# Kernel tuning notes

Measured on AMD Instinct MI355X. Metric: run time of the kernel, lower is better.

Reference implementation:

```python
import jax, jax.numpy as jnp
import numpy as np

N_NODES = 40000
N_EDGES = 640000
N_FEAT = 128
HIDDEN = 128
N_GRAPHS = 64


def _sage_conv(x, src, dst, Wl, b, Wr):
    # PyG SAGEConv (aggr='mean', root_weight=True, normalize=False):
    # out_i = W_l @ mean_{j in N(i)} x_j + b + W_r @ x_i
    msg = x[src]                                             # [E, F]
    s = jax.ops.segment_sum(msg, dst, num_segments=N_NODES)  # [N, F]
    deg = jax.ops.segment_sum(jnp.ones((src.shape[0],), x.dtype), dst,
                              num_segments=N_NODES)
    agg = s / jnp.maximum(deg, 1.0)[:, None]
    return agg @ Wl + b + x @ Wr


def setup_inputs() -> dict:
    key = jax.random.key(0)
    ks = jax.random.split(key, 12)
    sc = 1.0 / np.sqrt(N_FEAT)
    x = jax.random.normal(ks[0], (N_NODES, N_FEAT), dtype=jnp.float32)
    edge_index = jax.random.randint(ks[1], (2, N_EDGES), 0, N_NODES, dtype=jnp.int32)
    batch = jnp.sort(jax.random.randint(ks[2], (N_NODES,), 0, N_GRAPHS, dtype=jnp.int32))
    mk = lambda k, shp: (jax.random.normal(k, shp, dtype=jnp.float32) * sc)
    return {
        'x': x, 'edge_index': edge_index, 'batch': batch,
        'W1l': mk(ks[3], (N_FEAT, HIDDEN)), 'b1': jnp.zeros((HIDDEN,), jnp.float32),
        'W1r': mk(ks[4], (N_FEAT, HIDDEN)),
        'W2l': mk(ks[5], (HIDDEN, HIDDEN)), 'b2': jnp.zeros((HIDDEN,), jnp.float32),
        'W2r': mk(ks[6], (HIDDEN, HIDDEN)),
        'W3l': mk(ks[7], (HIDDEN, HIDDEN)), 'b3': jnp.zeros((HIDDEN,), jnp.float32),
        'W3r': mk(ks[8], (HIDDEN, HIDDEN)),
        'Wlin': mk(ks[9], (3 * HIDDEN, HIDDEN)), 'blin': jnp.zeros((HIDDEN,), jnp.float32),
    }


def reference(x, edge_index, batch, W1l, b1, W1r, W2l, b2, W2r, W3l, b3, W3r, Wlin, blin):
    src, dst = edge_index[0], edge_index[1]
    h1 = jax.nn.relu(_sage_conv(x, src, dst, W1l, b1, W1r))
    h2 = jax.nn.relu(_sage_conv(h1, src, dst, W2l, b2, W2r))
    h3 = jax.nn.relu(_sage_conv(h2, src, dst, W3l, b3, W3r))
    h = jnp.concatenate([h1, h2, h3], axis=1)                # [N, 3*H]
    pooled = jax.ops.segment_sum(h, batch, num_segments=N_GRAPHS)  # global_add_pool
    out = jax.nn.relu(pooled @ Wlin + blin)                  # [G, H]
    return out
```

## Files before the change

kernel.cpp:

```cpp
#include <hip/hip_runtime.h>
#include <hip/hip_bf16.h>

#define N_NODES 40000
#define N_EDGES 640000
#define NFEAT 128
#define NGRAPHS 64
#define ECAP 1536

typedef __attribute__((ext_vector_type(8))) short short8;
typedef __attribute__((ext_vector_type(4))) float float4v;

static __device__ __forceinline__ float bf2f(unsigned short u) {
    unsigned int x = ((unsigned int)u) << 16;
    return __builtin_bit_cast(float, x);
}
static __device__ __forceinline__ unsigned short f2bf(float f) {
    unsigned int x = __builtin_bit_cast(unsigned int, f);
    unsigned int r = x + 0x7fffu + ((x >> 16) & 1u);
    return (unsigned short)(r >> 16);
}

__global__ void k_prep(const int* __restrict__ dst, int* __restrict__ deg,
                       const int* __restrict__ batch, int* __restrict__ goff,
                       const float* __restrict__ x, unsigned short* __restrict__ h0,
                       const float* __restrict__ Wl0, const float* __restrict__ Wr0,
                       const float* __restrict__ Wl1, const float* __restrict__ Wr1,
                       const float* __restrict__ Wl2, const float* __restrict__ Wr2,
                       unsigned short* __restrict__ Wt) {
    int b = blockIdx.x;
    if (b < 2500) {
        int e = b * 256 + threadIdx.x;
        if (e < N_EDGES) atomicAdd(&deg[dst[e]], 1);
    } else if (b < 2657) {
        int i = (b - 2500) * 256 + threadIdx.x;
        if (i >= N_NODES) return;
        int b1 = batch[i];
        int b0 = (i == 0) ? -1 : batch[i - 1];
        for (int g = b0 + 1; g <= b1; ++g) goff[g] = i;
        if (i == N_NODES - 1)
            for (int g = b1 + 1; g <= NGRAPHS; ++g) goff[g] = N_NODES;
    } else if (b < 12657) {
        int i = (b - 2657) * 256 + threadIdx.x;
        const int n = N_NODES * NFEAT / 2;
        if (i < n) {
            float a = x[2 * i], c = x[2 * i + 1];
            unsigned int u = (unsigned int)f2bf(a) | ((unsigned int)f2bf(c) << 16);
            ((unsigned int*)h0)[i] = u;
        }
    } else {
        int id = (b - 12657) * 256 + threadIdx.x;
        if (id >= 3 * 128 * 256) return;
        int l   = id >> 15;
        int rem = id & 32767;
        int nn  = rem >> 8;
        int k   = rem & 255;
        const float* Wl = (l == 0) ? Wl0 : (l == 1) ? Wl1 : Wl2;
        const float* Wr = (l == 0) ? Wr0 : (l == 1) ? Wr1 : Wr2;
        float v = (k < 128) ? Wl[k * 128 + nn] : Wr[(k - 128) * 128 + nn];
        Wt[id] = f2bf(v);
    }
}

__global__ __launch_bounds__(1024) void k_scan1(const int* __restrict__ deg,
                                                int* __restrict__ offsets,
                                                int* __restrict__ bsum) {
    __shared__ int ws[16];
    int tid = threadIdx.x;
    int i = blockIdx.x * 1024 + tid;
    int v = (i < N_NODES) ? deg[i] : 0;
    int lane = tid & 63, wave = tid >> 6;
    int incl = v;
    for (int d = 1; d < 64; d <<= 1) {
        int t = __shfl_up(incl, d, 64);
        if (lane >= d) incl += t;
    }
    if (lane == 63) ws[wave] = incl;
    __syncthreads();
    if (wave == 0 && lane < 16) {
        int w = ws[lane];
        for (int d = 1; d < 16; d <<= 1) {
            int t = __shfl_up(w, d, 64);
            if (lane >= d) w += t;
        }
        ws[lane] = w;
    }
    __syncthreads();
    int waveOff = (wave == 0) ? 0 : ws[wave - 1];
    if (i < N_NODES) offsets[i] = waveOff + incl - v;
    if (tid == 1023) bsum[blockIdx.x] = ws[15];
}

__global__ __launch_bounds__(1024) void k_scan3(const int* __restrict__ bsum,
                                                int* __restrict__ offsets,
                                                int* __restrict__ cursor) {
    __shared__ int s_boff;
    int tid = threadIdx.x;
    if (tid < 64) {
        int v = (tid < 40) ? bsum[tid] : 0;
        int incl = v;
        for (int d = 1; d < 64; d <<= 1) {
            int t = __shfl_up(incl, d, 64);
            if (tid >= d) incl += t;
        }
        int excl = incl - v;
        int my = __shfl(excl, blockIdx.x, 64);
        if (tid == 0) s_boff = my;
    }
    __syncthreads();
    int boff = s_boff;
    int i = blockIdx.x * 1024 + tid;
    if (i < N_NODES) {
        int o = offsets[i] + boff;
        offsets[i] = o;
        cursor[i]  = o;
    }
    if (blockIdx.x == 0 && tid == 0) offsets[N_NODES] = N_EDGES;
}

__global__ void k_fill(const int* __restrict__ src, const int* __restrict__ dst,
                       int* __restrict__ cursor, int* __restrict__ esrc) {
    int e = blockIdx.x * 256 + threadIdx.x;
    if (e < N_EDGES) {
        int d = dst[e];
        int p = atomicAdd(&cursor[d], 1);
        esrc[p] = src[e];
    }
}

__global__ __launch_bounds__(256) void k_sage(
        const unsigned short* __restrict__ hin,
        const int* __restrict__ offsets,
        const int* __restrict__ esrc,
        const unsigned short* __restrict__ Wt,
        const float* __restrict__ bias,
        unsigned short* __restrict__ hout) {
    __shared__ __align__(16) unsigned short As[64][136];
    __shared__ int eidx[ECAP];
    int tid = threadIdx.x;
    int row0 = blockIdx.x * 64;

    int estart = offsets[row0];
    int ecnt   = offsets[row0 + 64] - estart;
    int staged = ecnt < ECAP ? ecnt : ECAP;

    for (int t = tid; t < staged; t += 256) eidx[t] = esrc[estart + t];
    __syncthreads();

    {
        int grp = tid >> 4;
        int sub = tid & 15;
        for (int nn = 0; nn < 4; ++nn) {
            int r = nn * 16 + grp;
            int node = row0 + r;
            int beg = offsets[node], end = offsets[node + 1];
            float a[8];
            for (int i = 0; i < 8; ++i) a[i] = 0.f;
            auto acc8 = [&](uint4 u) {
                a[0] += bf2f((unsigned short)(u.x & 0xffffu));
                a[1] += bf2f((unsigned short)(u.x >> 16));
                a[2] += bf2f((unsigned short)(u.y & 0xffffu));
                a[3] += bf2f((unsigned short)(u.y >> 16));
                a[4] += bf2f((unsigned short)(u.z & 0xffffu));
                a[5] += bf2f((unsigned short)(u.z >> 16));
                a[6] += bf2f((unsigned short)(u.w & 0xffffu));
                a[7] += bf2f((unsigned short)(u.w >> 16));
            };
            if (end - estart <= staged) {
                int lj = beg - estart, lend = end - estart;
                for (; lj + 8 <= lend; lj += 8) {
                    int s0 = eidx[lj],     s1 = eidx[lj + 1];
                    int s2 = eidx[lj + 2], s3 = eidx[lj + 3];
                    int s4 = eidx[lj + 4], s5 = eidx[lj + 5];
                    int s6 = eidx[lj + 6], s7 = eidx[lj + 7];
                    uint4 u0 = *(const uint4*)(hin + (size_t)s0 * 128 + sub * 8);
                    uint4 u1 = *(const uint4*)(hin + (size_t)s1 * 128 + sub * 8);
                    uint4 u2 = *(const uint4*)(hin + (size_t)s2 * 128 + sub * 8);
                    uint4 u3 = *(const uint4*)(hin + (size_t)s3 * 128 + sub * 8);
                    uint4 u4 = *(const uint4*)(hin + (size_t)s4 * 128 + sub * 8);
                    uint4 u5 = *(const uint4*)(hin + (size_t)s5 * 128 + sub * 8);
                    uint4 u6 = *(const uint4*)(hin + (size_t)s6 * 128 + sub * 8);
                    uint4 u7 = *(const uint4*)(hin + (size_t)s7 * 128 + sub * 8);
                    acc8(u0); acc8(u1); acc8(u2); acc8(u3);
                    acc8(u4); acc8(u5); acc8(u6); acc8(u7);
                }
                for (; lj < lend; ++lj) {
                    int s = eidx[lj];
                    uint4 u = *(const uint4*)(hin + (size_t)s * 128 + sub * 8);
                    acc8(u);
                }
            } else {
                for (int j = beg; j < end; ++j) {
                    int s = esrc[j];
                    uint4 u = *(const uint4*)(hin + (size_t)s * 128 + sub * 8);
                    acc8(u);
                }
            }
            int deg = end - beg;
            float inv = 1.f / (float)(deg > 1 ? deg : 1);
            uint4 v;
            v.x = (unsigned int)f2bf(a[0] * inv) | ((unsigned int)f2bf(a[1] * inv) << 16);
            v.y = (unsigned int)f2bf(a[2] * inv) | ((unsigned int)f2bf(a[3] * inv) << 16);
            v.z = (unsigned int)f2bf(a[4] * inv) | ((unsigned int)f2bf(a[5] * inv) << 16);
            v.w = (unsigned int)f2bf(a[6] * inv) | ((unsigned int)f2bf(a[7] * inv) << 16);
            *(uint4*)(&As[r][sub * 8]) = v;
        }
    }

    int wave = tid >> 6, lane = tid & 63;
    int quad = lane >> 4, l16 = lane & 15;
    float4v acc[4][2];
    for (int rt = 0; rt < 4; ++rt)
        for (int ct = 0; ct < 2; ++ct) acc[rt][ct] = {0.f, 0.f, 0.f, 0.f};

    int ncol0 = wave * 32;

    for (int kc = 0; kc < 4; ++kc) {
        int kg = kc * 32 + quad * 8;
        short8 a[4], b[2];
        for (int rt = 0; rt < 4; ++rt)
            a[rt] = *(const short8*)(hin + (size_t)(row0 + rt * 16 + l16) * 128 + kg);
        for (int ct = 0; ct < 2; ++ct)
            b[ct] = *(const short8*)(Wt + (size_t)(ncol0 + ct * 16 + l16) * 256 + 128 + kg);
        for (int rt = 0; rt < 4; ++rt)
            for (int ct = 0; ct < 2; ++ct)
                acc[rt][ct] = __builtin_amdgcn_mfma_f32_16x16x32_bf16(
                    a[rt], b[ct], acc[rt][ct], 0, 0, 0);
    }

    __syncthreads();

    for (int kc = 0; kc < 4; ++kc) {
        int k0 = kc * 32 + quad * 8;
        short8 a[4], b[2];
        for (int rt = 0; rt < 4; ++rt)
            a[rt] = *(const short8*)(&As[rt * 16 + l16][k0]);
        for (int ct = 0; ct < 2; ++ct)
            b[ct] = *(const short8*)(Wt + (size_t)(ncol0 + ct * 16 + l16) * 256 + k0);
        for (int rt = 0; rt < 4; ++rt)
            for (int ct = 0; ct < 2; ++ct)
                acc[rt][ct] = __builtin_amdgcn_mfma_f32_16x16x32_bf16(
                    a[rt], b[ct], acc[rt][ct], 0, 0, 0);
    }

    for (int ct = 0; ct < 2; ++ct) {
        int col = ncol0 + ct * 16 + l16;
        float bv = bias[col];
        for (int rt = 0; rt < 4; ++rt) {
            int r0 = rt * 16 + quad * 4;
            for (int i = 0; i < 4; ++i) {
                float v = acc[rt][ct][i] + bv;
                v = v > 0.f ? v : 0.f;
                hout[(size_t)(row0 + r0 + i) * 128 + col] = f2bf(v);
            }
        }
    }
}

__global__ __launch_bounds__(256) void k_pool(const unsigned short* __restrict__ h1,
                                              const unsigned short* __restrict__ h2,
                                              const unsigned short* __restrict__ h3,
                                              const int* __restrict__ goff,
                                              float* __restrict__ pooled) {
    __shared__ float red[4][16][8];
    int b = blockIdx.x;
    int g = b / 3, aidx = b % 3;
    const unsigned short* h = (aidx == 0) ? h1 : (aidx == 1) ? h2 : h3;
    int beg = goff[g], end = goff[g + 1];
    int tid = threadIdx.x;
    int rp = tid >> 4;
    int ch = tid & 15;
    float a[8];
    for (int i = 0; i < 8; ++i) a[i] = 0.f;
    for (int r = beg + rp; r < end; r += 16) {
        uint4 u = *(const uint4*)(h + (size_t)r * 128 + ch * 8);
        a[0] += bf2f((unsigned short)(u.x & 0xffffu));
        a[1] += bf2f((unsigned short)(u.x >> 16));
        a[2] += bf2f((unsigned short)(u.y & 0xffffu));
        a[3] += bf2f((unsigned short)(u.y >> 16));
        a[4] += bf2f((unsigned short)(u.z & 0xffffu));
        a[5] += bf2f((unsigned short)(u.z >> 16));
        a[6] += bf2f((unsigned short)(u.w & 0xffffu));
        a[7] += bf2f((unsigned short)(u.w >> 16));
    }
    for (int i = 0; i < 8; ++i) {
        a[i] += __shfl_xor(a[i], 16, 64);
        a[i] += __shfl_xor(a[i], 32, 64);
    }
    int wave = tid >> 6, lane = tid & 63;
    if (lane < 16)
        for (int i = 0; i < 8; ++i) red[wave][lane][i] = a[i];
    __syncthreads();
    if (tid < 128) {
        int ch2 = tid >> 3, e = tid & 7;
        float s = red[0][ch2][e] + red[1][ch2][e] + red[2][ch2][e] + red[3][ch2][e];
        pooled[g * 384 + aidx * 128 + ch2 * 8 + e] = s;
    }
}

__global__ void k_final(const float* __restrict__ pooled,
                        const float* __restrict__ Wlin,
                        const float* __restrict__ blin,
                        float* __restrict__ out) {
    int g = blockIdx.x, col = threadIdx.x;
    float acc = blin[col];
    for (int k = 0; k < 384; ++k)
        acc = fmaf(pooled[g * 384 + k], Wlin[k * 128 + col], acc);
    out[g * 128 + col] = acc > 0.f ? acc : 0.f;
}

extern "C" void kernel_launch(void* const* d_in, const int* in_sizes, int n_in,
                              void* d_out, int out_size, void* d_ws, size_t ws_size,
                              hipStream_t stream) {
    const float* x    = (const float*)d_in[0];
    const int*   ei   = (const int*)d_in[1];
    const int*   src  = ei;
    const int*   dst  = ei + N_EDGES;
    const int*   batch = (const int*)d_in[2];
    const float* W1l = (const float*)d_in[3];
    const float* b1  = (const float*)d_in[4];
    const float* W1r = (const float*)d_in[5];
    const float* W2l = (const float*)d_in[6];
    const float* b2  = (const float*)d_in[7];
    const float* W2r = (const float*)d_in[8];
    const float* W3l = (const float*)d_in[9];
    const float* b3  = (const float*)d_in[10];
    const float* W3r = (const float*)d_in[11];
    const float* Wlin = (const float*)d_in[12];
    const float* blin = (const float*)d_in[13];
    float* out = (float*)d_out;

    char* ws = (char*)d_ws;
    size_t off = 0;
    auto alloc = [&](size_t bytes) -> char* {
        char* p = ws + off;
        off = (off + bytes + 255) & ~(size_t)255;
        return p;
    };
    int* offsets = (int*)alloc((N_NODES + 1) * sizeof(int));
    int* cursor  = (int*)alloc(N_NODES * sizeof(int));
    int* deg     = (int*)alloc(N_NODES * sizeof(int));
    int* bsum    = (int*)alloc(64 * sizeof(int));
    int* goff    = (int*)alloc((NGRAPHS + 1) * sizeof(int));
    int* esrc    = (int*)alloc(N_EDGES * sizeof(int));
    unsigned short* h0   = (unsigned short*)alloc((size_t)N_NODES * 128 * 2);
    unsigned short* h1   = (unsigned short*)alloc((size_t)N_NODES * 128 * 2);
    unsigned short* h2   = (unsigned short*)alloc((size_t)N_NODES * 128 * 2);
    unsigned short* h3   = (unsigned short*)alloc((size_t)N_NODES * 128 * 2);
    unsigned short* Wt   = (unsigned short*)alloc(3 * 256 * 128 * 2);
    float* pooled = (float*)alloc(NGRAPHS * 384 * sizeof(float));

    hipMemsetAsync(deg, 0, N_NODES * sizeof(int), stream);

    k_prep<<<13041, 256, 0, stream>>>(dst, deg, batch, goff, x, h0,
                                      W1l, W1r, W2l, W2r, W3l, W3r, Wt);
    k_scan1<<<40, 1024, 0, stream>>>(deg, offsets, bsum);
    k_scan3<<<40, 1024, 0, stream>>>(bsum, offsets, cursor);
    k_fill<<<(N_EDGES + 255) / 256, 256, 0, stream>>>(src, dst, cursor, esrc);

    k_sage<<<625, 256, 0, stream>>>(h0, offsets, esrc, Wt,             b1, h1);
    k_sage<<<625, 256, 0, stream>>>(h1, offsets, esrc, Wt + 32768,     b2, h2);
    k_sage<<<625, 256, 0, stream>>>(h2, offsets, esrc, Wt + 2 * 32768, b3, h3);

    k_pool<<<3 * NGRAPHS, 256, 0, stream>>>(h1, h2, h3, goff, pooled);
    k_final<<<NGRAPHS, 128, 0, stream>>>(pooled, Wlin, blin, out);
}
```

Baseline: 283.6 us.

## Fuse scan kernels, stage root features in LDS, fuse pool with final linear

```diff
diff --git a/kernel.cpp b/kernel.cpp
--- a/kernel.cpp
+++ b/kernel.cpp
@@ -61,19 +61,37 @@
     }
 }
 
-__global__ __launch_bounds__(1024) void k_scan1(const int* __restrict__ deg,
-                                                int* __restrict__ offsets,
-                                                int* __restrict__ bsum) {
+__global__ __launch_bounds__(1024) void k_scan(const int* __restrict__ deg,
+                                               int* __restrict__ offsets,
+                                               int* __restrict__ cursor) {
     __shared__ int ws[16];
+    __shared__ int s_boff;
     int tid = threadIdx.x;
-    int i = blockIdx.x * 1024 + tid;
+    int b = blockIdx.x;
+    int lane = tid & 63, wave = tid >> 6;
+
+    int lim = b << 10;
+    int s = 0;
+    for (int i = tid; i < lim; i += 1024) s += deg[i];
+    for (int d = 1; d < 64; d <<= 1) s += __shfl_xor(s, d, 64);
+    if (lane == 0) ws[wave] = s;
+    __syncthreads();
+    if (tid == 0) {
+        int t = 0;
+        for (int w = 0; w < 16; ++w) t += ws[w];
+        s_boff = t;
+    }
+    __syncthreads();
+    int boff = s_boff;
+
+    int i = (b << 10) + tid;
     int v = (i < N_NODES) ? deg[i] : 0;
-    int lane = tid & 63, wave = tid >> 6;
     int incl = v;
     for (int d = 1; d < 64; d <<= 1) {
         int t = __shfl_up(incl, d, 64);
         if (lane >= d) incl += t;
     }
+    __syncthreads();
     if (lane == 63) ws[wave] = incl;
     __syncthreads();
     if (wave == 0 && lane < 16) {
@@ -86,35 +104,12 @@
     }
     __syncthreads();
     int waveOff = (wave == 0) ? 0 : ws[wave - 1];
-    if (i < N_NODES) offsets[i] = waveOff + incl - v;
-    if (tid == 1023) bsum[blockIdx.x] = ws[15];
-}
-
-__global__ __launch_bounds__(1024) void k_scan3(const int* __restrict__ bsum,
-                                                int* __restrict__ offsets,
-                                                int* __restrict__ cursor) {
-    __shared__ int s_boff;
-    int tid = threadIdx.x;
-    if (tid < 64) {
-        int v = (tid < 40) ? bsum[tid] : 0;
-        int incl = v;
-        for (int d = 1; d < 64; d <<= 1) {
-            int t = __shfl_up(incl, d, 64);
-            if (tid >= d) incl += t;
-        }
-        int excl = incl - v;
-        int my = __shfl(excl, blockIdx.x, 64);
-        if (tid == 0) s_boff = my;
-    }
-    __syncthreads();
-    int boff = s_boff;
-    int i = blockIdx.x * 1024 + tid;
     if (i < N_NODES) {
-        int o = offsets[i] + boff;
+        int o = boff + waveOff + incl - v;
         offsets[i] = o;
         cursor[i]  = o;
     }
-    if (blockIdx.x == 0 && tid == 0) offsets[N_NODES] = N_EDGES;
+    if (b == 39 && tid == 0) offsets[N_NODES] = N_EDGES;
 }
 
 __global__ void k_fill(const int* __restrict__ src, const int* __restrict__ dst,
@@ -134,7 +129,7 @@
         const unsigned short* __restrict__ Wt,
         const float* __restrict__ bias,
         unsigned short* __restrict__ hout) {
-    __shared__ __align__(16) unsigned short As[64][136];
+    __shared__ __align__(16) unsigned short As[64][264];
     __shared__ int eidx[ECAP];
     int tid = threadIdx.x;
     int row0 = blockIdx.x * 64;
@@ -143,6 +138,12 @@
     int ecnt   = offsets[row0 + 64] - estart;
     int staged = ecnt < ECAP ? ecnt : ECAP;
 
+    for (int p = 0; p < 4; ++p) {
+        int ci = tid + p * 256;
+        int r = ci >> 4, c8 = ci & 15;
+        uint4 v = *(const uint4*)(hin + (size_t)(row0 + r) * 128 + c8 * 8);
+        *(uint4*)(&As[r][128 + c8 * 8]) = v;
+    }
     for (int t = tid; t < staged; t += 256) eidx[t] = esrc[estart + t];
     __syncthreads();
 
@@ -205,6 +206,7 @@
             *(uint4*)(&As[r][sub * 8]) = v;
         }
     }
+    __syncthreads();
 
     int wave = tid >> 6, lane = tid & 63;
     int quad = lane >> 4, l16 = lane & 15;
@@ -213,23 +215,7 @@
         for (int ct = 0; ct < 2; ++ct) acc[rt][ct] = {0.f, 0.f, 0.f, 0.f};
 
     int ncol0 = wave * 32;
-
-    for (int kc = 0; kc < 4; ++kc) {
-        int kg = kc * 32 + quad * 8;
-        short8 a[4], b[2];
-        for (int rt = 0; rt < 4; ++rt)
-            a[rt] = *(const short8*)(hin + (size_t)(row0 + rt * 16 + l16) * 128 + kg);
-        for (int ct = 0; ct < 2; ++ct)
-            b[ct] = *(const short8*)(Wt + (size_t)(ncol0 + ct * 16 + l16) * 256 + 128 + kg);
-        for (int rt = 0; rt < 4; ++rt)
-            for (int ct = 0; ct < 2; ++ct)
-                acc[rt][ct] = __builtin_amdgcn_mfma_f32_16x16x32_bf16(
-                    a[rt], b[ct], acc[rt][ct], 0, 0, 0);
-    }
-
-    __syncthreads();
-
-    for (int kc = 0; kc < 4; ++kc) {
+    for (int kc = 0; kc < 8; ++kc) {
         int k0 = kc * 32 + quad * 8;
         short8 a[4], b[2];
         for (int rt = 0; rt < 4; ++rt)
@@ -256,56 +242,59 @@
     }
 }
 
-__global__ __launch_bounds__(256) void k_pool(const unsigned short* __restrict__ h1,
-                                              const unsigned short* __restrict__ h2,
-                                              const unsigned short* __restrict__ h3,
-                                              const int* __restrict__ goff,
-                                              float* __restrict__ pooled) {
+__global__ __launch_bounds__(256) void k_poolfinal(
+        const unsigned short* __restrict__ h1,
+        const unsigned short* __restrict__ h2,
+        const unsigned short* __restrict__ h3,
+        const int* __restrict__ goff,
+        const float* __restrict__ Wlin,
+        const float* __restrict__ blin,
+        float* __restrict__ out) {
     __shared__ float red[4][16][8];
-    int b = blockIdx.x;
-    int g = b / 3, aidx = b % 3;
-    const unsigned short* h = (aidx == 0) ? h1 : (aidx == 1) ? h2 : h3;
+    __shared__ float pool_s[384];
+    int g = blockIdx.x;
     int beg = goff[g], end = goff[g + 1];
     int tid = threadIdx.x;
     int rp = tid >> 4;
     int ch = tid & 15;
-    float a[8];
-    for (int i = 0; i < 8; ++i) a[i] = 0.f;
-    for (int r = beg + rp; r < end; r += 16) {
-        uint4 u = *(const uint4*)(h + (size_t)r * 128 + ch * 8);
-        a[0] += bf2f((unsigned short)(u.x & 0xffffu));
-        a[1] += bf2f((unsigned short)(u.x >> 16));
-        a[2] += bf2f((unsigned short)(u.y & 0xffffu));
-        a[3] += bf2f((unsigned short)(u.y >> 16));
-        a[4] += bf2f((unsigned short)(u.z & 0xffffu));
-        a[5] += bf2f((unsigned short)(u.z >> 16));
-        a[6] += bf2f((unsigned short)(u.w & 0xffffu));
-        a[7] += bf2f((unsigned short)(u.w >> 16));
-    }
-    for (int i = 0; i < 8; ++i) {
-        a[i] += __shfl_xor(a[i], 16, 64);
-        a[i] += __shfl_xor(a[i], 32, 64);
-    }
     int wave = tid >> 6, lane = tid & 63;
-    if (lane < 16)
-        for (int i = 0; i < 8; ++i) red[wave][lane][i] = a[i];
-    __syncthreads();
+
+    for (int aidx = 0; aidx < 3; ++aidx) {
+        const unsigned short* h = (aidx == 0) ? h1 : (aidx == 1) ? h2 : h3;
+        float a[8];
+        for (int i = 0; i < 8; ++i) a[i] = 0.f;
+        for (int r = beg + rp; r < end; r += 16) {
+            uint4 u = *(const uint4*)(h + (size_t)r * 128 + ch * 8);
+            a[0] += bf2f((unsigned short)(u.x & 0xffffu));
+            a[1] += bf2f((unsigned short)(u.x >> 16));
+            a[2] += bf2f((unsigned short)(u.y & 0xffffu));
+            a[3] += bf2f((unsigned short)(u.y >> 16));
+            a[4] += bf2f((unsigned short)(u.z & 0xffffu));
+            a[5] += bf2f((unsigned short)(u.z >> 16));
+            a[6] += bf2f((unsigned short)(u.w & 0xffffu));
+            a[7] += bf2f((unsigned short)(u.w >> 16));
+        }
+        for (int i = 0; i < 8; ++i) {
+            a[i] += __shfl_xor(a[i], 16, 64);
+            a[i] += __shfl_xor(a[i], 32, 64);
+        }
+        if (lane < 16)
+            for (int i = 0; i < 8; ++i) red[wave][lane][i] = a[i];
+        __syncthreads();
+        if (tid < 128) {
+            int ch2 = tid >> 3, e = tid & 7;
+            pool_s[aidx * 128 + ch2 * 8 + e] =
+                red[0][ch2][e] + red[1][ch2][e] + red[2][ch2][e] + red[3][ch2][e];
+        }
+        __syncthreads();
+    }
+
     if (tid < 128) {
-        int ch2 = tid >> 3, e = tid & 7;
-        float s = red[0][ch2][e] + red[1][ch2][e] + red[2][ch2][e] + red[3][ch2][e];
-        pooled[g * 384 + aidx * 128 + ch2 * 8 + e] = s;
-    }
-}
-
-__global__ void k_final(const float* __restrict__ pooled,
-                        const float* __restrict__ Wlin,
-                        const float* __restrict__ blin,
-                        float* __restrict__ out) {
-    int g = blockIdx.x, col = threadIdx.x;
-    float acc = blin[col];
-    for (int k = 0; k < 384; ++k)
-        acc = fmaf(pooled[g * 384 + k], Wlin[k * 128 + col], acc);
-    out[g * 128 + col] = acc > 0.f ? acc : 0.f;
+        float acc = blin[tid];
+        for (int k = 0; k < 384; ++k)
+            acc = fmaf(pool_s[k], Wlin[k * 128 + tid], acc);
+        out[g * 128 + tid] = acc > 0.f ? acc : 0.f;
+    }
 }
 
 extern "C" void kernel_launch(void* const* d_in, const int* in_sizes, int n_in,
@@ -339,7 +328,6 @@
     int* offsets = (int*)alloc((N_NODES + 1) * sizeof(int));
     int* cursor  = (int*)alloc(N_NODES * sizeof(int));
     int* deg     = (int*)alloc(N_NODES * sizeof(int));
-    int* bsum    = (int*)alloc(64 * sizeof(int));
     int* goff    = (int*)alloc((NGRAPHS + 1) * sizeof(int));
     int* esrc    = (int*)alloc(N_EDGES * sizeof(int));
     unsigned short* h0   = (unsigned short*)alloc((size_t)N_NODES * 128 * 2);
@@ -347,20 +335,17 @@
     unsigned short* h2   = (unsigned short*)alloc((size_t)N_NODES * 128 * 2);
     unsigned short* h3   = (unsigned short*)alloc((size_t)N_NODES * 128 * 2);
     unsigned short* Wt   = (unsigned short*)alloc(3 * 256 * 128 * 2);
-    float* pooled = (float*)alloc(NGRAPHS * 384 * sizeof(float));
 
     hipMemsetAsync(deg, 0, N_NODES * sizeof(int), stream);
 
     k_prep<<<13041, 256, 0, stream>>>(dst, deg, batch, goff, x, h0,
                                       W1l, W1r, W2l, W2r, W3l, W3r, Wt);
-    k_scan1<<<40, 1024, 0, stream>>>(deg, offsets, bsum);
-    k_scan3<<<40, 1024, 0, stream>>>(bsum, offsets, cursor);
+    k_scan<<<40, 1024, 0, stream>>>(deg, offsets, cursor);
     k_fill<<<(N_EDGES + 255) / 256, 256, 0, stream>>>(src, dst, cursor, esrc);
 
     k_sage<<<625, 256, 0, stream>>>(h0, offsets, esrc, Wt,             b1, h1);
     k_sage<<<625, 256, 0, stream>>>(h1, offsets, esrc, Wt + 32768,     b2, h2);
     k_sage<<<625, 256, 0, stream>>>(h2, offsets, esrc, Wt + 2 * 32768, b3, h3);
 
-    k_pool<<<3 * NGRAPHS, 256, 0, stream>>>(h1, h2, h3, goff, pooled);
-    k_final<<<NGRAPHS, 128, 0, stream>>>(pooled, Wlin, blin, out);
-}
+    k_poolfinal<<<NGRAPHS, 256, 0, stream>>>(h1, h2, h3, goff, Wlin, blin, out);
+}
```

After: 297.9 us. +5.1%, slower.
